# Performance work log

Measured on AMD Instinct MI355X. Metric: run time of the kernel, lower is better.

## Reference

```python
import jax, jax.numpy as jnp
import numpy as np

B, C = 65536, 512  # entity pairs x relation classes (class 0 = threshold class)
NEG_BIG = 1e30


def setup_inputs() -> dict:
    key = jax.random.key(0)
    k1, k2 = jax.random.split(key)
    logits = jax.random.normal(k1, (B, C), dtype=jnp.float32)
    # sparse multi-hot labels; column 0 is the threshold class (zeroed in forward anyway)
    labels = (jax.random.uniform(k2, (B, C)) < 0.03).astype(jnp.float32)
    return {"logits": logits, "labels": labels}


def reference(logits, labels):
    # th_label has 1 only in column 0; labels have column 0 forced to 0
    labels = labels.at[:, 0].set(0.0)
    pos_count = labels.sum(axis=1)                         # [B] number of positive labels per row
    row_mask = (pos_count > 0).astype(logits.dtype)        # rows contributing to loss1

    # loss1: for each positive row, log(1 - sigmoid(logit_0)) + sum_{j: label=1} log(sigmoid(logit_j)),
    # averaged over the total number of such terms. log(1-sigmoid(x)) == log_sigmoid(-x).
    term = jax.nn.log_sigmoid(-logits[:, 0]) + (labels * jax.nn.log_sigmoid(logits)).sum(axis=1)
    count = (row_mask * (1.0 + pos_count)).sum()
    loss1 = -(row_mask * term).sum() / count

    # loss2: mask out positive-label logits, then -log_softmax at the threshold class
    logit2 = logits - labels * NEG_BIG
    loss2 = -jax.nn.log_softmax(logit2, axis=-1)[:, 0]     # [B]

    return loss1 + loss2.mean()
```

## Files before the change

kernel.cpp:

```cpp
#include <hip/hip_runtime.h>

constexpr int Bn = 65536;
constexpr int Cn = 512;

#define L2E 1.4426950408889634f
#define LN2 0.6931471805599453f

typedef float f32x4 __attribute__((ext_vector_type(4)));

__device__ __forceinline__ void gl2lds16(const float* g, float* l) {
  __builtin_amdgcn_global_load_lds(
      (const __attribute__((address_space(1))) void*)g,
      (__attribute__((address_space(3))) void*)l, 16, 0, 0);
}

__device__ __forceinline__ uint32_t lds_addr(const void* p) {
  return (uint32_t)(uintptr_t)(__attribute__((address_space(3))) const char*)(const char*)p;
}

template <int Ctrl, int RowMask>
__device__ __forceinline__ float dpp_get(float x, float ident) {
  return __int_as_float(__builtin_amdgcn_update_dpp(
      __float_as_int(ident), __float_as_int(x), Ctrl, RowMask, 0xf, false));
}

__global__ __launch_bounds__(256, 2) void matloss_main(
    const float* __restrict__ logits,
    const float* __restrict__ labels,
    double* __restrict__ acc) {

  const int lane = threadIdx.x & 63;
  const int wib  = threadIdx.x >> 6;
  const int gw   = blockIdx.x * 4 + wib;
  constexpr int IT = 16;
  const size_t row0 = (size_t)gw * 32;

  __shared__ float smem[4 * 2 * 2048];
  float* slot0 = &smem[wib * 4096];
  float* slot1 = slot0 + 2048;

  auto stage = [&](int i, float* slot) {
#pragma unroll
    for (int r = 0; r < 2; ++r) {
      const size_t row = row0 + 2 * i + r;
      const float* gl = logits + row * Cn + lane * 4;
      const float* gb = labels + row * Cn + lane * 4;
      float* s = slot + r * 1024;
      gl2lds16(gl,       s);
      gl2lds16(gl + 256, s + 256);
      gl2lds16(gb,       s + 512);
      gl2lds16(gb + 256, s + 768);
    }
  };

  stage(0, slot0);
  stage(1, slot1);

  const uint32_t a0 = lds_addr(slot0) + lane * 16;
  const uint32_t a1 = a0 + 8192;

  float a_term = 0.f, a_cnt = 0.f, a_l2 = 0.f;

#pragma unroll
  for (int i = 0; i < IT; ++i) {
    if (i == IT - 1) asm volatile("s_waitcnt vmcnt(0)" ::: "memory");
    else             asm volatile("s_waitcnt vmcnt(8)" ::: "memory");
    __builtin_amdgcn_sched_barrier(0);

    f32x4 q[8];
    const uint32_t va = (i & 1) ? a1 : a0;
    asm volatile("ds_read_b128 %0, %8\n\t"
                 "ds_read_b128 %1, %8 offset:1024\n\t"
                 "ds_read_b128 %2, %8 offset:2048\n\t"
                 "ds_read_b128 %3, %8 offset:3072\n\t"
                 "ds_read_b128 %4, %8 offset:4096\n\t"
                 "ds_read_b128 %5, %8 offset:5120\n\t"
                 "ds_read_b128 %6, %8 offset:6144\n\t"
                 "ds_read_b128 %7, %8 offset:7168"
                 : "=&v"(q[0]), "=&v"(q[1]), "=&v"(q[2]), "=&v"(q[3]),
                   "=&v"(q[4]), "=&v"(q[5]), "=&v"(q[6]), "=&v"(q[7])
                 : "v"(va));
    asm volatile("s_waitcnt lgkmcnt(0)" ::: "memory");
    __builtin_amdgcn_sched_barrier(0);

    if (i + 2 < IT) stage(i + 2, (i & 1) ? slot1 : slot0);

    float P[2], S[2], PM[2], CN[2], xz[2];
#pragma unroll
    for (int r = 0; r < 2; ++r) {
      f32x4 xa = q[4 * r], xb = q[4 * r + 1], la = q[4 * r + 2], lc = q[4 * r + 3];
      float x[8] = {xa.x, xa.y, xa.z, xa.w, xb.x, xb.y, xb.z, xb.w};
      float l[8] = {la.x, la.y, la.z, la.w, lc.x, lc.y, lc.z, lc.w};
      xz[r] = __int_as_float(__builtin_amdgcn_readfirstlane(__float_as_int(x[0])));
      if (lane == 0) l[0] = 0.f;

      float Pr = 1.f, Sr = 0.f, PMr = 0.f, CNr = 0.f;
#pragma unroll
      for (int k = 0; k < 8; ++k) {
        bool  pos = (l[k] != 0.f);
        float sel = pos ? -fabsf(x[k]) : x[k];
        float e   = __builtin_amdgcn_exp2f(sel * L2E);
        Pr  *= fmaf(l[k], e, 1.f);
        Sr  += pos ? 0.f : e;
        PMr  = fmaf(l[k], fminf(x[k], 0.f), PMr);
        CNr += l[k];
      }
      P[r] = Pr; S[r] = Sr; PM[r] = PMr; CN[r] = CNr;
    }

#define RED8(CTRL, RM)                                        \
    _Pragma("unroll")                                         \
    for (int r = 0; r < 2; ++r) {                             \
      S[r]  += dpp_get<CTRL, RM>(S[r],  0.f);                 \
      CN[r] += dpp_get<CTRL, RM>(CN[r], 0.f);                 \
      PM[r] += dpp_get<CTRL, RM>(PM[r], 0.f);                 \
      P[r]  *= dpp_get<CTRL, RM>(P[r],  1.f);                 \
    }
    RED8(0x111, 0xf)
    RED8(0x112, 0xf)
    RED8(0x114, 0xf)
    RED8(0x118, 0xf)
    RED8(0x142, 0xa)
    RED8(0x143, 0xc)
#undef RED8

#pragma unroll
    for (int r = 0; r < 2; ++r) {
      float Sw  = __int_as_float(__builtin_amdgcn_readlane(__float_as_int(S[r]),  63));
      float CNw = __int_as_float(__builtin_amdgcn_readlane(__float_as_int(CN[r]), 63));
      float PMw = __int_as_float(__builtin_amdgcn_readlane(__float_as_int(PM[r]), 63));
      float Pw  = __int_as_float(__builtin_amdgcn_readlane(__float_as_int(P[r]),  63));

      a_l2 += LN2 * __builtin_amdgcn_logf(Sw) - xz[r];
      if (CNw > 0.f) {
        float t0  = __builtin_amdgcn_exp2f(-fabsf(xz[r]) * L2E);
        float ls0 = fminf(-xz[r], 0.f) - LN2 * __builtin_amdgcn_logf(1.f + t0);
        a_term += ls0 + PMw - LN2 * __builtin_amdgcn_logf(Pw);
        a_cnt  += 1.f + CNw;
      }
    }
  }

  __syncthreads();
  if (lane == 0) { smem[wib] = a_term; smem[4 + wib] = a_cnt; smem[8 + wib] = a_l2; }
  __syncthreads();
  if (threadIdx.x == 0) {
    atomicAdd(&acc[0], (double)(smem[0] + smem[1] + smem[2]  + smem[3]));
    atomicAdd(&acc[1], (double)(smem[4] + smem[5] + smem[6]  + smem[7]));
    atomicAdd(&acc[2], (double)(smem[8] + smem[9] + smem[10] + smem[11]));
  }
}

__global__ void matloss_final(const double* __restrict__ acc, float* __restrict__ out) {
  out[0] = (float)(-acc[0] / acc[1] + acc[2] / (double)Bn);
}

extern "C" void kernel_launch(void* const* d_in, const int* in_sizes, int n_in,
                              void* d_out, int out_size, void* d_ws, size_t ws_size,
                              hipStream_t stream) {
  const float* logits = (const float*)d_in[0];
  const float* labels = (const float*)d_in[1];
  float* out = (float*)d_out;
  double* acc = (double*)d_ws;

  hipMemsetAsync(d_ws, 0, 3 * sizeof(double), stream);
  matloss_main<<<512, 256, 0, stream>>>(logits, labels, acc);
  matloss_final<<<1, 1, 0, stream>>>(acc, out);
}
```

Baseline: 60.54 us.

## Process four rows per wave iteration with two-wave blocks and deeper staging

Each wave now handles 64 rows, four per iteration instead of two, so there are half as many waves (512 blocks of 2 waves). The LDS double buffer per wave doubles, each step issues twice as many async global-to-LDS loads, and the wait threshold is raised to match. The aim is more bytes in flight per wave and less fixed per-iteration overhead for the reductions and waits. In exchange the kernel uses more registers and LDS per wave and runs far fewer waves, which may leave HBM bandwidth underused on a memory-bound kernel.

```diff
diff --git a/kernel.cpp b/kernel.cpp
--- a/kernel.cpp
+++ b/kernel.cpp
@@ -24,25 +24,25 @@
       __float_as_int(ident), __float_as_int(x), Ctrl, RowMask, 0xf, false));
 }
 
-__global__ __launch_bounds__(256, 2) void matloss_main(
+__global__ __launch_bounds__(128) void matloss_main(
     const float* __restrict__ logits,
     const float* __restrict__ labels,
     double* __restrict__ acc) {
 
   const int lane = threadIdx.x & 63;
   const int wib  = threadIdx.x >> 6;
-  const int gw   = blockIdx.x * 4 + wib;
+  const int gw   = blockIdx.x * 2 + wib;
   constexpr int IT = 16;
-  const size_t row0 = (size_t)gw * 32;
+  const size_t row0 = (size_t)gw * 64;
 
-  __shared__ float smem[4 * 2 * 2048];
-  float* slot0 = &smem[wib * 4096];
-  float* slot1 = slot0 + 2048;
+  __shared__ float smem[2 * 2 * 4096];
+  float* slot0 = &smem[wib * 8192];
+  float* slot1 = slot0 + 4096;
 
   auto stage = [&](int i, float* slot) {
 #pragma unroll
-    for (int r = 0; r < 2; ++r) {
-      const size_t row = row0 + 2 * i + r;
+    for (int r = 0; r < 4; ++r) {
+      const size_t row = row0 + 4 * i + r;
       const float* gl = logits + row * Cn + lane * 4;
       const float* gb = labels + row * Cn + lane * 4;
       float* s = slot + r * 1024;
@@ -57,37 +57,48 @@
   stage(1, slot1);
 
   const uint32_t a0 = lds_addr(slot0) + lane * 16;
-  const uint32_t a1 = a0 + 8192;
+  const uint32_t a1 = a0 + 16384;
 
   float a_term = 0.f, a_cnt = 0.f, a_l2 = 0.f;
 
 #pragma unroll
   for (int i = 0; i < IT; ++i) {
     if (i == IT - 1) asm volatile("s_waitcnt vmcnt(0)" ::: "memory");
-    else             asm volatile("s_waitcnt vmcnt(8)" ::: "memory");
+    else             asm volatile("s_waitcnt vmcnt(16)" ::: "memory");
     __builtin_amdgcn_sched_barrier(0);
 
-    f32x4 q[8];
+    f32x4 q[16];
     const uint32_t va = (i & 1) ? a1 : a0;
-    asm volatile("ds_read_b128 %0, %8\n\t"
-                 "ds_read_b128 %1, %8 offset:1024\n\t"
-                 "ds_read_b128 %2, %8 offset:2048\n\t"
-                 "ds_read_b128 %3, %8 offset:3072\n\t"
-                 "ds_read_b128 %4, %8 offset:4096\n\t"
-                 "ds_read_b128 %5, %8 offset:5120\n\t"
-                 "ds_read_b128 %6, %8 offset:6144\n\t"
-                 "ds_read_b128 %7, %8 offset:7168"
-                 : "=&v"(q[0]), "=&v"(q[1]), "=&v"(q[2]), "=&v"(q[3]),
-                   "=&v"(q[4]), "=&v"(q[5]), "=&v"(q[6]), "=&v"(q[7])
-                 : "v"(va));
+    asm volatile(
+        "ds_read_b128 %0,  %16\n\t"
+        "ds_read_b128 %1,  %16 offset:1024\n\t"
+        "ds_read_b128 %2,  %16 offset:2048\n\t"
+        "ds_read_b128 %3,  %16 offset:3072\n\t"
+        "ds_read_b128 %4,  %16 offset:4096\n\t"
+        "ds_read_b128 %5,  %16 offset:5120\n\t"
+        "ds_read_b128 %6,  %16 offset:6144\n\t"
+        "ds_read_b128 %7,  %16 offset:7168\n\t"
+        "ds_read_b128 %8,  %16 offset:8192\n\t"
+        "ds_read_b128 %9,  %16 offset:9216\n\t"
+        "ds_read_b128 %10, %16 offset:10240\n\t"
+        "ds_read_b128 %11, %16 offset:11264\n\t"
+        "ds_read_b128 %12, %16 offset:12288\n\t"
+        "ds_read_b128 %13, %16 offset:13312\n\t"
+        "ds_read_b128 %14, %16 offset:14336\n\t"
+        "ds_read_b128 %15, %16 offset:15360"
+        : "=&v"(q[0]),  "=&v"(q[1]),  "=&v"(q[2]),  "=&v"(q[3]),
+          "=&v"(q[4]),  "=&v"(q[5]),  "=&v"(q[6]),  "=&v"(q[7]),
+          "=&v"(q[8]),  "=&v"(q[9]),  "=&v"(q[10]), "=&v"(q[11]),
+          "=&v"(q[12]), "=&v"(q[13]), "=&v"(q[14]), "=&v"(q[15])
+        : "v"(va));
     asm volatile("s_waitcnt lgkmcnt(0)" ::: "memory");
     __builtin_amdgcn_sched_barrier(0);
 
     if (i + 2 < IT) stage(i + 2, (i & 1) ? slot1 : slot0);
 
-    float P[2], S[2], PM[2], CN[2], xz[2];
+    float P[4], S[4], PM[4], CN[4], xz[4];
 #pragma unroll
-    for (int r = 0; r < 2; ++r) {
+    for (int r = 0; r < 4; ++r) {
       f32x4 xa = q[4 * r], xb = q[4 * r + 1], la = q[4 * r + 2], lc = q[4 * r + 3];
       float x[8] = {xa.x, xa.y, xa.z, xa.w, xb.x, xb.y, xb.z, xb.w};
       float l[8] = {la.x, la.y, la.z, la.w, lc.x, lc.y, lc.z, lc.w};
@@ -108,24 +119,24 @@
       P[r] = Pr; S[r] = Sr; PM[r] = PMr; CN[r] = CNr;
     }
 
-#define RED8(CTRL, RM)                                        \
+#define RED16(CTRL, RM)                                       \
     _Pragma("unroll")                                         \
-    for (int r = 0; r < 2; ++r) {                             \
+    for (int r = 0; r < 4; ++r) {                             \
       S[r]  += dpp_get<CTRL, RM>(S[r],  0.f);                 \
       CN[r] += dpp_get<CTRL, RM>(CN[r], 0.f);                 \
       PM[r] += dpp_get<CTRL, RM>(PM[r], 0.f);                 \
       P[r]  *= dpp_get<CTRL, RM>(P[r],  1.f);                 \
     }
-    RED8(0x111, 0xf)
-    RED8(0x112, 0xf)
-    RED8(0x114, 0xf)
-    RED8(0x118, 0xf)
-    RED8(0x142, 0xa)
-    RED8(0x143, 0xc)
-#undef RED8
+    RED16(0x111, 0xf)
+    RED16(0x112, 0xf)
+    RED16(0x114, 0xf)
+    RED16(0x118, 0xf)
+    RED16(0x142, 0xa)
+    RED16(0x143, 0xc)
+#undef RED16
 
 #pragma unroll
-    for (int r = 0; r < 2; ++r) {
+    for (int r = 0; r < 4; ++r) {
       float Sw  = __int_as_float(__builtin_amdgcn_readlane(__float_as_int(S[r]),  63));
       float CNw = __int_as_float(__builtin_amdgcn_readlane(__float_as_int(CN[r]), 63));
       float PMw = __int_as_float(__builtin_amdgcn_readlane(__float_as_int(PM[r]), 63));
@@ -142,12 +153,12 @@
   }
 
   __syncthreads();
-  if (lane == 0) { smem[wib] = a_term; smem[4 + wib] = a_cnt; smem[8 + wib] = a_l2; }
+  if (lane == 0) { smem[wib] = a_term; smem[2 + wib] = a_cnt; smem[4 + wib] = a_l2; }
   __syncthreads();
   if (threadIdx.x == 0) {
-    atomicAdd(&acc[0], (double)(smem[0] + smem[1] + smem[2]  + smem[3]));
-    atomicAdd(&acc[1], (double)(smem[4] + smem[5] + smem[6]  + smem[7]));
-    atomicAdd(&acc[2], (double)(smem[8] + smem[9] + smem[10] + smem[11]));
+    atomicAdd(&acc[0], (double)(smem[0] + smem[1]));
+    atomicAdd(&acc[1], (double)(smem[2] + smem[3]));
+    atomicAdd(&acc[2], (double)(smem[4] + smem[5]));
   }
 }
 
@@ -164,6 +175,6 @@
   double* acc = (double*)d_ws;
 
   hipMemsetAsync(d_ws, 0, 3 * sizeof(double), stream);
-  matloss_main<<<512, 256, 0, stream>>>(logits, labels, acc);
+  matloss_main<<<512, 128, 0, stream>>>(logits, labels, acc);
   matloss_final<<<1, 1, 0, stream>>>(acc, out);
 }
```

Result: slower. 69.52 us (+14.8%).

## Use single-wave blocks with balanced row-pair split across 2560 waves

Applied to the files above, without the earlier changes.

Each block is now one 64-thread wave instead of four, and the grid is 2560 blocks. Each wave handles 13 or 12 row pairs so that 32768 pairs are spread evenly over 2560 waves, one wave per SIMD across the MI355X's 256 CUs. The aim is to fix the tail imbalance of 2048 waves each doing 16 pairs. The block-level LDS reduction is replaced by per-wave double atomics, which adds 2560 atomics per accumulator. The loop is no longer fully unrolled because its trip count is now a runtime value.

```diff
diff --git a/kernel.cpp b/kernel.cpp
--- a/kernel.cpp
+++ b/kernel.cpp
@@ -24,25 +24,25 @@
       __float_as_int(ident), __float_as_int(x), Ctrl, RowMask, 0xf, false));
 }
 
-__global__ __launch_bounds__(256, 2) void matloss_main(
+__global__ __launch_bounds__(64, 3) void matloss_main(
     const float* __restrict__ logits,
     const float* __restrict__ labels,
     double* __restrict__ acc) {
 
   const int lane = threadIdx.x & 63;
-  const int wib  = threadIdx.x >> 6;
-  const int gw   = blockIdx.x * 4 + wib;
-  constexpr int IT = 16;
-  const size_t row0 = (size_t)gw * 32;
+  const int w    = blockIdx.x;
+  const int n    = (w < 2048) ? 13 : 12;
+  const size_t pstart = (w < 2048) ? (size_t)w * 13
+                                   : 26624 + (size_t)(w - 2048) * 12;
 
-  __shared__ float smem[4 * 2 * 2048];
-  float* slot0 = &smem[wib * 4096];
-  float* slot1 = slot0 + 2048;
+  __shared__ float smem[4096];
+  float* slot0 = smem;
+  float* slot1 = smem + 2048;
 
-  auto stage = [&](int i, float* slot) {
+  auto stage = [&](size_t p, float* slot) {
 #pragma unroll
     for (int r = 0; r < 2; ++r) {
-      const size_t row = row0 + 2 * i + r;
+      const size_t row = 2 * p + r;
       const float* gl = logits + row * Cn + lane * 4;
       const float* gb = labels + row * Cn + lane * 4;
       float* s = slot + r * 1024;
@@ -53,18 +53,17 @@
     }
   };
 
-  stage(0, slot0);
-  stage(1, slot1);
+  stage(pstart,     slot0);
+  stage(pstart + 1, slot1);
 
   const uint32_t a0 = lds_addr(slot0) + lane * 16;
   const uint32_t a1 = a0 + 8192;
 
   float a_term = 0.f, a_cnt = 0.f, a_l2 = 0.f;
 
-#pragma unroll
-  for (int i = 0; i < IT; ++i) {
-    if (i == IT - 1) asm volatile("s_waitcnt vmcnt(0)" ::: "memory");
-    else             asm volatile("s_waitcnt vmcnt(8)" ::: "memory");
+  for (int i = 0; i < n; ++i) {
+    if (i == n - 1) asm volatile("s_waitcnt vmcnt(0)" ::: "memory");
+    else            asm volatile("s_waitcnt vmcnt(8)" ::: "memory");
     __builtin_amdgcn_sched_barrier(0);
 
     f32x4 q[8];
@@ -83,7 +82,7 @@
     asm volatile("s_waitcnt lgkmcnt(0)" ::: "memory");
     __builtin_amdgcn_sched_barrier(0);
 
-    if (i + 2 < IT) stage(i + 2, (i & 1) ? slot1 : slot0);
+    if (i + 2 < n) stage(pstart + i + 2, (i & 1) ? slot1 : slot0);
 
     float P[2], S[2], PM[2], CN[2], xz[2];
 #pragma unroll
@@ -141,13 +140,10 @@
     }
   }
 
-  __syncthreads();
-  if (lane == 0) { smem[wib] = a_term; smem[4 + wib] = a_cnt; smem[8 + wib] = a_l2; }
-  __syncthreads();
-  if (threadIdx.x == 0) {
-    atomicAdd(&acc[0], (double)(smem[0] + smem[1] + smem[2]  + smem[3]));
-    atomicAdd(&acc[1], (double)(smem[4] + smem[5] + smem[6]  + smem[7]));
-    atomicAdd(&acc[2], (double)(smem[8] + smem[9] + smem[10] + smem[11]));
+  if (lane == 0) {
+    atomicAdd(&acc[0], (double)a_term);
+    atomicAdd(&acc[1], (double)a_cnt);
+    atomicAdd(&acc[2], (double)a_l2);
   }
 }
 
@@ -164,6 +160,6 @@
   double* acc = (double*)d_ws;
 
   hipMemsetAsync(d_ws, 0, 3 * sizeof(double), stream);
-  matloss_main<<<512, 256, 0, stream>>>(logits, labels, acc);
+  matloss_main<<<2560, 64, 0, stream>>>(logits, labels, acc);
   matloss_final<<<1, 1, 0, stream>>>(acc, out);
 }
```

Result: slower. 132.7 us (+119.2%).
